# Kernel tuning notes

Measured on AMD Instinct MI355X. Metric: run time of the kernel, lower is better.

The kernel has to match this reference:

```python
import jax, jax.numpy as jnp
import numpy as np

N_NODES = 50000


def _gcn_layer(x, src, dst, W, b, inv_deg):
    # gather src features, scatter-add into dst, right-normalize, then dense transform
    agg = jax.ops.segment_sum(x[src], dst, num_segments=N_NODES)  # [N, F]
    h = agg * inv_deg[:, None]
    return h @ W + b


def setup_inputs() -> dict:
    key = jax.random.key(0)
    ks = jax.random.split(key, 6)
    E = 800000
    x = jax.random.normal(ks[0], (N_NODES, 128), dtype=jnp.float32)
    src = jax.random.randint(ks[1], (E,), 0, N_NODES, dtype=jnp.int64)
    dst = jax.random.randint(ks[2], (E,), 0, N_NODES, dtype=jnp.int64)
    W1 = jax.random.normal(ks[3], (128, 128), dtype=jnp.float32) * (1.0 / np.sqrt(128))
    b1 = jnp.zeros((128,), dtype=jnp.float32)
    W2 = jax.random.normal(ks[4], (128, 64), dtype=jnp.float32) * (1.0 / np.sqrt(128))
    b2 = jnp.zeros((64,), dtype=jnp.float32)
    return {"x": x, "src": src, "dst": dst, "W1": W1, "b1": b1, "W2": W2, "b2": b2}


def reference(x, src, dst, W1, b1, W2, b2):
    # in-degree, clamped to 1 (DGL norm='right')
    deg = jax.ops.segment_sum(jnp.ones_like(dst, dtype=x.dtype), dst, num_segments=N_NODES)
    inv_deg = 1.0 / jnp.maximum(deg, 1.0)
    h = _gcn_layer(x, src, dst, W1, b1, inv_deg)
    h = jax.nn.relu(h)  # Dropout in eval mode == identity
    out = _gcn_layer(h, src, dst, W2, b2, inv_deg)
    return out
```

## Files before the change

### kernel.cpp

```cpp
#include <hip/hip_runtime.h>


constexpr int NNODES = 50000;
constexpr int NEDGES = 800000;
constexpr int SCAN_BLOCKS = (NNODES + 255) / 256;
constexpr int ABLOCKS = 200;
constexpr int PER = (NEDGES + ABLOCKS - 1) / ABLOCKS;

typedef unsigned short ushortv8 __attribute__((ext_vector_type(8)));
typedef short bf16x8 __attribute__((ext_vector_type(8)));
typedef float f32x4 __attribute__((ext_vector_type(4)));

static __device__ __forceinline__ unsigned short f2bf(float f) {
    unsigned u = __float_as_uint(f);
    u += 0x7fff + ((u >> 16) & 1);
    return (unsigned short)(u >> 16);
}
static __device__ __forceinline__ float bf2f(unsigned short h) {
    return __uint_as_float((unsigned)h << 16);
}

__global__ __launch_bounds__(256) void partA_kernel(
    const int* __restrict__ src, const int* __restrict__ dst,
    unsigned* __restrict__ tmp, int* __restrict__ H,
    int* __restrict__ LOFS, int nE)
{
    __shared__ int cnt[256];
    __shared__ int ofs[256];
    __shared__ int cur[256];
    const int t = threadIdx.x;
    cnt[t] = 0;
    __syncthreads();
    const int lo = blockIdx.x * PER;
    const int hi = min(lo + PER, nE);
    for (int i = lo + t; i < hi; i += 256)
        atomicAdd(&cnt[dst[i] >> 8], 1);
    __syncthreads();
    ofs[t] = cnt[t];
    __syncthreads();
    #pragma unroll
    for (int off = 1; off < 256; off <<= 1) {
        const int o = (t >= off) ? ofs[t - off] : 0;
        __syncthreads();
        ofs[t] += o;
        __syncthreads();
    }
    const int excl = ofs[t] - cnt[t];
    cur[t] = excl;
    H[blockIdx.x * 256 + t] = cnt[t];
    LOFS[blockIdx.x * 256 + t] = excl;
    __syncthreads();
    for (int i = lo + t; i < hi; i += 256) {
        const int d = dst[i];
        const unsigned pk = ((unsigned)src[i] << 8) | (unsigned)(d & 255);
        const int pos = lo + atomicAdd(&cur[d >> 8], 1);
        tmp[pos] = pk;
    }
}

__global__ __launch_bounds__(256) void bucketScan_kernel(
    const int* __restrict__ H, int* __restrict__ bucketStart)
{
    __shared__ int s[256];
    const int t = threadIdx.x;
    int sum = 0;
    for (int w = 0; w < ABLOCKS; ++w) sum += H[w * 256 + t];
    s[t] = sum;
    __syncthreads();
    #pragma unroll
    for (int off = 1; off < 256; off <<= 1) {
        const int o = (t >= off) ? s[t - off] : 0;
        __syncthreads();
        s[t] += o;
        __syncthreads();
    }
    bucketStart[t] = s[t] - sum;
}

__global__ __launch_bounds__(256) void partB_kernel(
    const unsigned* __restrict__ tmp, const int* __restrict__ H,
    const int* __restrict__ LOFS, const int* __restrict__ bucketStart,
    int* __restrict__ csr, int* __restrict__ rowStart,
    float* __restrict__ inv_deg, int nNodes)
{
    __shared__ int pfx[ABLOCKS + 1];
    __shared__ int base[ABLOCKS];
    __shared__ int cnt[256];
    __shared__ int scn[256];
    __shared__ int fill[256];
    const int b = blockIdx.x;
    const int t = threadIdx.x;
    cnt[t] = 0;
    if (t < ABLOCKS) {
        pfx[t + 1] = H[t * 256 + b];
        base[t] = t * PER + LOFS[t * 256 + b];
    }
    if (t == 0) pfx[0] = 0;
    __syncthreads();
    if (t == 0) {
        int run = 0;
        for (int w = 0; w < ABLOCKS; ++w) { run += pfx[w + 1]; pfx[w + 1] = run; }
    }
    __syncthreads();
    const int total = pfx[ABLOCKS];
    for (int j = t; j < total; j += 256) {
        int loW = 0, hiW = ABLOCKS;
        while (hiW - loW > 1) {
            const int mid = (loW + hiW) >> 1;
            if (pfx[mid] <= j) loW = mid; else hiW = mid;
        }
        const unsigned p = tmp[base[loW] + (j - pfx[loW])];
        atomicAdd(&cnt[p & 255u], 1);
    }
    __syncthreads();
    scn[t] = cnt[t];
    __syncthreads();
    #pragma unroll
    for (int off = 1; off < 256; off <<= 1) {
        const int o = (t >= off) ? scn[t - off] : 0;
        __syncthreads();
        scn[t] += o;
        __syncthreads();
    }
    const int gbase = bucketStart[b];
    const int excl = gbase + scn[t] - cnt[t];
    const int node = b * 256 + t;
    if (node < nNodes) {
        rowStart[node] = excl;
        inv_deg[node] = 1.0f / fmaxf((float)cnt[t], 1.0f);
    }
    if (b == 0 && t == 0) rowStart[nNodes] = NEDGES;
    fill[t] = excl;
    __syncthreads();
    for (int j = t; j < total; j += 256) {
        int loW = 0, hiW = ABLOCKS;
        while (hiW - loW > 1) {
            const int mid = (loW + hiW) >> 1;
            if (pfx[mid] <= j) loW = mid; else hiW = mid;
        }
        const unsigned p = tmp[base[loW] + (j - pfx[loW])];
        const int pos = atomicAdd(&fill[p & 255u], 1);
        csr[pos] = (int)(p >> 8);
    }
}

__global__ __launch_bounds__(256) void cast_kernel(
    const float* __restrict__ in, ushortv8* __restrict__ outh, int n8)
{
    int i = blockIdx.x * 256 + threadIdx.x;
    if (i >= n8) return;
    const float4* p = reinterpret_cast<const float4*>(in) + (size_t)i * 2;
    const float4 a = p[0], b = p[1];
    ushortv8 v;
    v[0] = f2bf(a.x); v[1] = f2bf(a.y); v[2] = f2bf(a.z); v[3] = f2bf(a.w);
    v[4] = f2bf(b.x); v[5] = f2bf(b.y); v[6] = f2bf(b.z); v[7] = f2bf(b.w);
    outh[i] = v;
}

__global__ __launch_bounds__(256) void prep_kernel(
    const float* __restrict__ W1, const float* __restrict__ W2,
    unsigned short* __restrict__ Wt1, unsigned short* __restrict__ Wt2)
{
    const int i = blockIdx.x * 256 + threadIdx.x;
    if (i < 128 * 128) {
        const int n = i >> 7, k = i & 127;
        Wt1[i] = f2bf(W1[k * 128 + n]);
    } else if (i < 128 * 128 + 64 * 128) {
        const int j = i - 128 * 128;
        const int n = j >> 7, k = j & 127;
        Wt2[j] = f2bf(W2[k * 64 + n]);
    }
}

template<int F, bool EPI, bool OBF16>
__global__ __launch_bounds__(256) void gather_bf16_kernel(
    const ushortv8* __restrict__ feat, const int* __restrict__ csr,
    const int* __restrict__ rowStart, const float* __restrict__ inv_deg,
    const float* __restrict__ bias, void* __restrict__ outv, int nNodes)
{
    constexpr int LPR = F / 8;
    constexpr int EPW = 64 / LPR;
    const int wid = (blockIdx.x * 256 + threadIdx.x) >> 6;
    if (wid >= nNodes) return;
    const int lane = threadIdx.x & 63;
    const int eslot = lane / LPR;
    const int cg = lane % LPR;
    const int rs = rowStart[wid];
    const int re = rowStart[wid + 1];

    float acc0[8] = {}, acc1[8] = {};
    int j = rs + eslot;
    for (; j + EPW < re; j += 2 * EPW) {
        const int s0 = csr[j];
        const int s1 = csr[j + EPW];
        const ushortv8 v0 = feat[(size_t)s0 * LPR + cg];
        const ushortv8 v1 = feat[(size_t)s1 * LPR + cg];
        #pragma unroll
        for (int t = 0; t < 8; ++t) acc0[t] += bf2f(v0[t]);
        #pragma unroll
        for (int t = 0; t < 8; ++t) acc1[t] += bf2f(v1[t]);
    }
    if (j < re) {
        const int s0 = csr[j];
        const ushortv8 v0 = feat[(size_t)s0 * LPR + cg];
        #pragma unroll
        for (int t = 0; t < 8; ++t) acc0[t] += bf2f(v0[t]);
    }
    #pragma unroll
    for (int t = 0; t < 8; ++t) acc0[t] += acc1[t];

    #pragma unroll
    for (int off = LPR; off < 64; off <<= 1) {
        #pragma unroll
        for (int t = 0; t < 8; ++t) acc0[t] += __shfl_down(acc0[t], off, 64);
    }

    if (lane < LPR) {
        if constexpr (EPI) {
            const float s = inv_deg[wid];
            #pragma unroll
            for (int t = 0; t < 8; ++t) acc0[t] = acc0[t] * s + bias[cg * 8 + t];
        }
        if constexpr (OBF16) {
            ushortv8 ov;
            #pragma unroll
            for (int t = 0; t < 8; ++t) ov[t] = f2bf(acc0[t]);
            *reinterpret_cast<ushortv8*>(
                (unsigned short*)outv + (size_t)wid * F + cg * 8) = ov;
        } else {
            float* o = (float*)outv + (size_t)wid * F + cg * 8;
            *reinterpret_cast<float4*>(o) =
                make_float4(acc0[0], acc0[1], acc0[2], acc0[3]);
            *reinterpret_cast<float4*>(o + 4) =
                make_float4(acc0[4], acc0[5], acc0[6], acc0[7]);
        }
    }
}

template<int OUT, bool SCALE, bool BIAS, bool RELU>
__global__ __launch_bounds__(256) void mfma_gemm_kernel(
    const ushortv8* __restrict__ A,
    const float* __restrict__ inv_deg,
    const ushortv8* __restrict__ Wt,
    const float* __restrict__ bias,
    unsigned short* __restrict__ outh,
    int nrows)
{
    constexpr int NT = OUT / 16;
    constexpr int LDK = 136;
    __shared__ alignas(16) unsigned short lwt[OUT][LDK];
    __shared__ alignas(16) unsigned short la[64][LDK];

    const int row0 = blockIdx.x * 64;
    const int t = threadIdx.x;

    for (int i = t; i < OUT * 16; i += 256) {
        const int r = i >> 4, c = i & 15;
        *reinterpret_cast<ushortv8*>(&lwt[r][c * 8]) = Wt[i];
    }
    for (int i = t; i < 64 * 16; i += 256) {
        const int r = i >> 4, c = i & 15;
        const int row = row0 + r;
        ushortv8 v = {};
        if (row < nrows) {
            v = A[(size_t)row * 16 + c];
            if constexpr (SCALE) {
                const float s = inv_deg[row];
                #pragma unroll
                for (int jj = 0; jj < 8; ++jj) v[jj] = f2bf(bf2f(v[jj]) * s);
            }
        }
        *reinterpret_cast<ushortv8*>(&la[r][c * 8]) = v;
    }
    __syncthreads();

    const int wave = t >> 6, lane = t & 63;
    const int m = lane & 15, kg = lane >> 4;

    f32x4 acc[NT] = {};
    #pragma unroll
    for (int kk = 0; kk < 4; ++kk) {
        const bf16x8 af =
            *reinterpret_cast<const bf16x8*>(&la[wave * 16 + m][kk * 32 + kg * 8]);
        #pragma unroll
        for (int n = 0; n < NT; ++n) {
            const bf16x8 bf =
                *reinterpret_cast<const bf16x8*>(&lwt[n * 16 + m][kk * 32 + kg * 8]);
            acc[n] = __builtin_amdgcn_mfma_f32_16x16x32_bf16(af, bf, acc[n], 0, 0, 0);
        }
    }

    __syncthreads();
    unsigned short* lo = &la[0][0];
    constexpr int LDO = OUT + 8;
    #pragma unroll
    for (int n = 0; n < NT; ++n) {
        float bv = 0.f;
        if constexpr (BIAS) bv = bias[n * 16 + m];
        #pragma unroll
        for (int q = 0; q < 4; ++q) {
            const int r = wave * 16 + kg * 4 + q;
            float v = acc[n][q] + bv;
            if constexpr (RELU) v = fmaxf(v, 0.f);
            lo[r * LDO + n * 16 + m] = f2bf(v);
        }
    }
    __syncthreads();
    for (int i = t; i < 64 * (OUT / 8); i += 256) {
        const int r = i / (OUT / 8), c = i % (OUT / 8);
        const int row = row0 + r;
        if (row < nrows)
            *reinterpret_cast<ushortv8*>(&outh[(size_t)row * OUT + c * 8]) =
                *reinterpret_cast<const ushortv8*>(&lo[r * LDO + c * 8]);
    }
}

extern "C" void kernel_launch(void* const* d_in, const int* in_sizes, int n_in,
                              void* d_out, int out_size, void* d_ws, size_t ws_size,
                              hipStream_t stream)
{
    const float* x   = (const float*)d_in[0];
    const int*   src = (const int*)d_in[1];
    const int*   dst = (const int*)d_in[2];
    const float* W1  = (const float*)d_in[3];
    const float* b1  = (const float*)d_in[4];
    const float* W2  = (const float*)d_in[5];
    const float* b2  = (const float*)d_in[6];
    float* out = (float*)d_out;

    float* ws  = (float*)d_ws;
    int*   wsi = (int*)d_ws;
    int*            rowStart    = wsi + 0;
    float*          invdeg      = ws  + 50048;
    int*            bucketStart = wsi + 100096;
    int*            H           = wsi + 100352;
    int*            LOFS        = wsi + 151552;
    int*            csr         = wsi + 202752;
    unsigned*       tmp         = (unsigned*)(wsi + 1002752);
    unsigned short* Wt1         = (unsigned short*)(wsi + 1802752);
    unsigned short* Wt2         = (unsigned short*)(wsi + 1810944);
    ushortv8*       xh          = (ushortv8*)(wsi + 1815040);
    ushortv8*       aggH        = (ushortv8*)(wsi + 5015040);
    ushortv8*       h           = (ushortv8*)(wsi + 6615040);
    ushortv8*       y2h         = (ushortv8*)(wsi + 8215040);

    partA_kernel<<<ABLOCKS, 256, 0, stream>>>(src, dst, tmp, H, LOFS, NEDGES);
    bucketScan_kernel<<<1, 256, 0, stream>>>(H, bucketStart);
    partB_kernel<<<SCAN_BLOCKS, 256, 0, stream>>>(
        tmp, H, LOFS, bucketStart, csr, rowStart, invdeg, NNODES);

    cast_kernel<<<(NNODES * 128 / 8 + 255) / 256, 256, 0, stream>>>(
        x, xh, NNODES * 128 / 8);
    prep_kernel<<<(128 * 128 + 64 * 128 + 255) / 256, 256, 0, stream>>>(
        W1, W2, Wt1, Wt2);

    gather_bf16_kernel<128, false, true><<<(NNODES + 3) / 4, 256, 0, stream>>>(
        xh, csr, rowStart, nullptr, nullptr, aggH, NNODES);
    mfma_gemm_kernel<128, true, true, true><<<(NNODES + 63) / 64, 256, 0, stream>>>(
        aggH, invdeg, (const ushortv8*)Wt1, b1, (unsigned short*)h, NNODES);

    mfma_gemm_kernel<64, false, false, false><<<(NNODES + 63) / 64, 256, 0, stream>>>(
        h, nullptr, (const ushortv8*)Wt2, nullptr, (unsigned short*)y2h, NNODES);
    gather_bf16_kernel<64, true, false><<<(NNODES + 3) / 4, 256, 0, stream>>>(
        y2h, csr, rowStart, invdeg, b2, out, NNODES);
}
```

Measured before the change: 137.8 us.

## Fuse setup kernels, fold bucket scan into partB, and fuse both GEMMs

Merges the edge partitioning, feature cast and weight transpose into one multi-role setup kernel. Every partB block now recomputes the global bucket scan redundantly instead of relying on a separate single-block kernel. The two dense GEMMs are fused so the hidden layer stays in LDS and is never written to or read back from global memory. Together these cut five launches down to two and remove a global round trip for the hidden layer. In exchange, each partB block re-reads the whole H histogram, and the fused GEMM uses more LDS per block.

```diff
diff --git a/kernel.cpp b/kernel.cpp
--- a/kernel.cpp
+++ b/kernel.cpp
@@ -3,9 +3,37 @@
 
 constexpr int NNODES = 50000;
 constexpr int NEDGES = 800000;
-constexpr int SCAN_BLOCKS = (NNODES + 255) / 256;
+constexpr int NBUCKETS = (NNODES + 255) / 256;
 constexpr int ABLOCKS = 200;
 constexpr int PER = (NEDGES + ABLOCKS - 1) / ABLOCKS;
+constexpr int NB_CAST = NNODES * 128 / 8 / 256;
+constexpr int NB_PREP = (128 * 128 + 64 * 128 + 255) / 256;
+
+constexpr size_t SZ_ROWSTART = 50048;
+constexpr size_t SZ_INVDEG   = 50048;
+constexpr size_t SZ_H        = (size_t)ABLOCKS * 256;
+constexpr size_t SZ_LOFS     = (size_t)ABLOCKS * 256;
+constexpr size_t SZ_CSR      = NEDGES;
+constexpr size_t SZ_TMP      = NEDGES;
+constexpr size_t SZ_WT1      = 128 * 128 / 2;
+constexpr size_t SZ_WT2      = 64 * 128 / 2;
+constexpr size_t SZ_XH       = (size_t)NNODES * 128 / 2;
+constexpr size_t SZ_AGGH     = (size_t)NNODES * 128 / 2;
+constexpr size_t SZ_Y2H      = (size_t)NNODES * 64 / 2;
+
+constexpr size_t OFF_ROWSTART = 0;
+constexpr size_t OFF_INVDEG   = OFF_ROWSTART + SZ_ROWSTART;
+constexpr size_t OFF_H        = OFF_INVDEG   + SZ_INVDEG;
+constexpr size_t OFF_LOFS     = OFF_H        + SZ_H;
+constexpr size_t OFF_CSR      = OFF_LOFS     + SZ_LOFS;
+constexpr size_t OFF_TMP      = OFF_CSR      + SZ_CSR;
+constexpr size_t OFF_WT1      = OFF_TMP      + SZ_TMP;
+constexpr size_t OFF_WT2      = OFF_WT1      + SZ_WT1;
+constexpr size_t OFF_XH       = OFF_WT2      + SZ_WT2;
+constexpr size_t OFF_AGGH     = OFF_XH       + SZ_XH;
+constexpr size_t OFF_Y2H      = OFF_AGGH     + SZ_AGGH;
+constexpr size_t WS_WORDS     = OFF_Y2H      + SZ_Y2H;
+static_assert(WS_WORDS < 11452800, "exceeds r7-proven workspace size");
 
 typedef unsigned short ushortv8 __attribute__((ext_vector_type(8)));
 typedef short bf16x8 __attribute__((ext_vector_type(8)));
@@ -20,110 +48,132 @@
     return __uint_as_float((unsigned)h << 16);
 }
 
-__global__ __launch_bounds__(256) void partA_kernel(
+__global__ __launch_bounds__(256) void setup_kernel(
     const int* __restrict__ src, const int* __restrict__ dst,
-    unsigned* __restrict__ tmp, int* __restrict__ H,
-    int* __restrict__ LOFS, int nE)
+    unsigned* __restrict__ tmp, int* __restrict__ H, int* __restrict__ LOFS,
+    const float* __restrict__ x, ushortv8* __restrict__ xh,
+    const float* __restrict__ W1, const float* __restrict__ W2,
+    unsigned short* __restrict__ Wt1, unsigned short* __restrict__ Wt2)
 {
-    __shared__ int cnt[256];
-    __shared__ int ofs[256];
-    __shared__ int cur[256];
+    const int blk = blockIdx.x;
     const int t = threadIdx.x;
-    cnt[t] = 0;
-    __syncthreads();
-    const int lo = blockIdx.x * PER;
-    const int hi = min(lo + PER, nE);
-    for (int i = lo + t; i < hi; i += 256)
-        atomicAdd(&cnt[dst[i] >> 8], 1);
-    __syncthreads();
-    ofs[t] = cnt[t];
-    __syncthreads();
-    #pragma unroll
-    for (int off = 1; off < 256; off <<= 1) {
-        const int o = (t >= off) ? ofs[t - off] : 0;
-        __syncthreads();
-        ofs[t] += o;
-        __syncthreads();
-    }
-    const int excl = ofs[t] - cnt[t];
-    cur[t] = excl;
-    H[blockIdx.x * 256 + t] = cnt[t];
-    LOFS[blockIdx.x * 256 + t] = excl;
-    __syncthreads();
-    for (int i = lo + t; i < hi; i += 256) {
-        const int d = dst[i];
-        const unsigned pk = ((unsigned)src[i] << 8) | (unsigned)(d & 255);
-        const int pos = lo + atomicAdd(&cur[d >> 8], 1);
-        tmp[pos] = pk;
-    }
-}
-
-__global__ __launch_bounds__(256) void bucketScan_kernel(
-    const int* __restrict__ H, int* __restrict__ bucketStart)
-{
-    __shared__ int s[256];
-    const int t = threadIdx.x;
-    int sum = 0;
-    for (int w = 0; w < ABLOCKS; ++w) sum += H[w * 256 + t];
-    s[t] = sum;
-    __syncthreads();
-    #pragma unroll
-    for (int off = 1; off < 256; off <<= 1) {
-        const int o = (t >= off) ? s[t - off] : 0;
-        __syncthreads();
-        s[t] += o;
-        __syncthreads();
-    }
-    bucketStart[t] = s[t] - sum;
+    if (blk < ABLOCKS) {
+        __shared__ int cnt[256];
+        __shared__ int ofs[256];
+        __shared__ int cur[256];
+        cnt[t] = 0;
+        __syncthreads();
+        const int lo = blk * PER;
+        const int hi = min(lo + PER, NEDGES);
+        for (int i = lo + t; i < hi; i += 256)
+            atomicAdd(&cnt[dst[i] >> 8], 1);
+        __syncthreads();
+        ofs[t] = cnt[t];
+        __syncthreads();
+        #pragma unroll
+        for (int off = 1; off < 256; off <<= 1) {
+            const int o = (t >= off) ? ofs[t - off] : 0;
+            __syncthreads();
+            ofs[t] += o;
+            __syncthreads();
+        }
+        const int excl = ofs[t] - cnt[t];
+        cur[t] = excl;
+        H[blk * 256 + t] = cnt[t];
+        LOFS[blk * 256 + t] = excl;
+        __syncthreads();
+        for (int i = lo + t; i < hi; i += 256) {
+            const int d = dst[i];
+            const unsigned pk = ((unsigned)src[i] << 8) | (unsigned)(d & 255);
+            const int pos = lo + atomicAdd(&cur[d >> 8], 1);
+            tmp[pos] = pk;
+        }
+    } else if (blk < ABLOCKS + NB_CAST) {
+        const int i = (blk - ABLOCKS) * 256 + t;
+        const float4* p = reinterpret_cast<const float4*>(x) + (size_t)i * 2;
+        const float4 a = p[0], b = p[1];
+        ushortv8 v;
+        v[0] = f2bf(a.x); v[1] = f2bf(a.y); v[2] = f2bf(a.z); v[3] = f2bf(a.w);
+        v[4] = f2bf(b.x); v[5] = f2bf(b.y); v[6] = f2bf(b.z); v[7] = f2bf(b.w);
+        xh[i] = v;
+    } else {
+        const int i = (blk - ABLOCKS - NB_CAST) * 256 + t;
+        if (i < 128 * 128) {
+            const int n = i >> 7, k = i & 127;
+            Wt1[i] = f2bf(W1[k * 128 + n]);
+        } else if (i < 128 * 128 + 64 * 128) {
+            const int j = i - 128 * 128;
+            const int n = j >> 7, k = j & 127;
+            Wt2[j] = f2bf(W2[k * 64 + n]);
+        }
+    }
 }
 
 __global__ __launch_bounds__(256) void partB_kernel(
     const unsigned* __restrict__ tmp, const int* __restrict__ H,
-    const int* __restrict__ LOFS, const int* __restrict__ bucketStart,
-    int* __restrict__ csr, int* __restrict__ rowStart,
-    float* __restrict__ inv_deg, int nNodes)
+    const int* __restrict__ LOFS, int* __restrict__ csr,
+    int* __restrict__ rowStart, float* __restrict__ inv_deg, int nNodes)
 {
-    __shared__ int pfx[ABLOCKS + 1];
-    __shared__ int base[ABLOCKS];
+    __shared__ int cs[256];
+    __shared__ int s[256];
+    __shared__ int epfx[256];
+    __shared__ int base[256];
     __shared__ int cnt[256];
-    __shared__ int scn[256];
     __shared__ int fill[256];
     const int b = blockIdx.x;
     const int t = threadIdx.x;
+
+    int sum = 0;
+    for (int w = 0; w < ABLOCKS; ++w) sum += H[w * 256 + t];
+    cs[t] = sum;
+    s[t] = sum;
+    __syncthreads();
+    #pragma unroll
+    for (int off = 1; off < 256; off <<= 1) {
+        const int o = (t >= off) ? s[t - off] : 0;
+        __syncthreads();
+        s[t] += o;
+        __syncthreads();
+    }
+    const int gbase = s[b] - cs[b];
+    const int total = cs[b];
+    __syncthreads();
+
+    const int hv = (t < ABLOCKS) ? H[t * 256 + b] : 0;
+    s[t] = hv;
+    if (t < ABLOCKS) base[t] = t * PER + LOFS[t * 256 + b];
     cnt[t] = 0;
-    if (t < ABLOCKS) {
-        pfx[t + 1] = H[t * 256 + b];
-        base[t] = t * PER + LOFS[t * 256 + b];
-    }
-    if (t == 0) pfx[0] = 0;
-    __syncthreads();
-    if (t == 0) {
-        int run = 0;
-        for (int w = 0; w < ABLOCKS; ++w) { run += pfx[w + 1]; pfx[w + 1] = run; }
-    }
-    __syncthreads();
-    const int total = pfx[ABLOCKS];
+    __syncthreads();
+    #pragma unroll
+    for (int off = 1; off < 256; off <<= 1) {
+        const int o = (t >= off) ? s[t - off] : 0;
+        __syncthreads();
+        s[t] += o;
+        __syncthreads();
+    }
+    epfx[t] = s[t] - hv;
+    __syncthreads();
+
     for (int j = t; j < total; j += 256) {
         int loW = 0, hiW = ABLOCKS;
         while (hiW - loW > 1) {
             const int mid = (loW + hiW) >> 1;
-            if (pfx[mid] <= j) loW = mid; else hiW = mid;
-        }
-        const unsigned p = tmp[base[loW] + (j - pfx[loW])];
+            if (epfx[mid] <= j) loW = mid; else hiW = mid;
+        }
+        const unsigned p = tmp[base[loW] + (j - epfx[loW])];
         atomicAdd(&cnt[p & 255u], 1);
     }
     __syncthreads();
-    scn[t] = cnt[t];
+    s[t] = cnt[t];
     __syncthreads();
     #pragma unroll
     for (int off = 1; off < 256; off <<= 1) {
-        const int o = (t >= off) ? scn[t - off] : 0;
-        __syncthreads();
-        scn[t] += o;
-        __syncthreads();
-    }
-    const int gbase = bucketStart[b];
-    const int excl = gbase + scn[t] - cnt[t];
+        const int o = (t >= off) ? s[t - off] : 0;
+        __syncthreads();
+        s[t] += o;
+        __syncthreads();
+    }
+    const int excl = gbase + s[t] - cnt[t];
     const int node = b * 256 + t;
     if (node < nNodes) {
         rowStart[node] = excl;
@@ -132,43 +182,16 @@
     if (b == 0 && t == 0) rowStart[nNodes] = NEDGES;
     fill[t] = excl;
     __syncthreads();
+
     for (int j = t; j < total; j += 256) {
         int loW = 0, hiW = ABLOCKS;
         while (hiW - loW > 1) {
             const int mid = (loW + hiW) >> 1;
-            if (pfx[mid] <= j) loW = mid; else hiW = mid;
-        }
-        const unsigned p = tmp[base[loW] + (j - pfx[loW])];
+            if (epfx[mid] <= j) loW = mid; else hiW = mid;
+        }
+        const unsigned p = tmp[base[loW] + (j - epfx[loW])];
         const int pos = atomicAdd(&fill[p & 255u], 1);
         csr[pos] = (int)(p >> 8);
-    }
-}
-
-__global__ __launch_bounds__(256) void cast_kernel(
-    const float* __restrict__ in, ushortv8* __restrict__ outh, int n8)
-{
-    int i = blockIdx.x * 256 + threadIdx.x;
-    if (i >= n8) return;
-    const float4* p = reinterpret_cast<const float4*>(in) + (size_t)i * 2;
-    const float4 a = p[0], b = p[1];
-    ushortv8 v;
-    v[0] = f2bf(a.x); v[1] = f2bf(a.y); v[2] = f2bf(a.z); v[3] = f2bf(a.w);
-    v[4] = f2bf(b.x); v[5] = f2bf(b.y); v[6] = f2bf(b.z); v[7] = f2bf(b.w);
-    outh[i] = v;
-}
-
-__global__ __launch_bounds__(256) void prep_kernel(
-    const float* __restrict__ W1, const float* __restrict__ W2,
-    unsigned short* __restrict__ Wt1, unsigned short* __restrict__ Wt2)
-{
-    const int i = blockIdx.x * 256 + threadIdx.x;
-    if (i < 128 * 128) {
-        const int n = i >> 7, k = i & 127;
-        Wt1[i] = f2bf(W1[k * 128 + n]);
-    } else if (i < 128 * 128 + 64 * 128) {
-        const int j = i - 128 * 128;
-        const int n = j >> 7, k = j & 127;
-        Wt2[j] = f2bf(W2[k * 64 + n]);
     }
 }
 
@@ -237,26 +260,30 @@
     }
 }
 
-template<int OUT, bool SCALE, bool BIAS, bool RELU>
-__global__ __launch_bounds__(256) void mfma_gemm_kernel(
+__global__ __launch_bounds__(256) void mfma_fused_kernel(
     const ushortv8* __restrict__ A,
     const float* __restrict__ inv_deg,
-    const ushortv8* __restrict__ Wt,
-    const float* __restrict__ bias,
-    unsigned short* __restrict__ outh,
+    const ushortv8* __restrict__ Wt1,
+    const float* __restrict__ b1,
+    const ushortv8* __restrict__ Wt2,
+    unsigned short* __restrict__ y2h,
     int nrows)
 {
-    constexpr int NT = OUT / 16;
     constexpr int LDK = 136;
-    __shared__ alignas(16) unsigned short lwt[OUT][LDK];
+    __shared__ alignas(16) unsigned short lwt1[128][LDK];
+    __shared__ alignas(16) unsigned short lwt2[64][LDK];
     __shared__ alignas(16) unsigned short la[64][LDK];
 
     const int row0 = blockIdx.x * 64;
     const int t = threadIdx.x;
 
-    for (int i = t; i < OUT * 16; i += 256) {
+    for (int i = t; i < 128 * 16; i += 256) {
         const int r = i >> 4, c = i & 15;
-        *reinterpret_cast<ushortv8*>(&lwt[r][c * 8]) = Wt[i];
+        *reinterpret_cast<ushortv8*>(&lwt1[r][c * 8]) = Wt1[i];
+    }
+    for (int i = t; i < 64 * 16; i += 256) {
+        const int r = i >> 4, c = i & 15;
+        *reinterpret_cast<ushortv8*>(&lwt2[r][c * 8]) = Wt2[i];
     }
     for (int i = t; i < 64 * 16; i += 256) {
         const int r = i >> 4, c = i & 15;
@@ -264,11 +291,9 @@
         ushortv8 v = {};
         if (row < nrows) {
             v = A[(size_t)row * 16 + c];
-            if constexpr (SCALE) {
-                const float s = inv_deg[row];
-                #pragma unroll
-                for (int jj = 0; jj < 8; ++jj) v[jj] = f2bf(bf2f(v[jj]) * s);
-            }
+            const float s = inv_deg[row];
+            #pragma unroll
+            for (int jj = 0; jj < 8; ++jj) v[jj] = f2bf(bf2f(v[jj]) * s);
         }
         *reinterpret_cast<ushortv8*>(&la[r][c * 8]) = v;
     }
@@ -277,41 +302,57 @@
     const int wave = t >> 6, lane = t & 63;
     const int m = lane & 15, kg = lane >> 4;
 
-    f32x4 acc[NT] = {};
+    f32x4 acc1[8] = {};
     #pragma unroll
     for (int kk = 0; kk < 4; ++kk) {
         const bf16x8 af =
             *reinterpret_cast<const bf16x8*>(&la[wave * 16 + m][kk * 32 + kg * 8]);
         #pragma unroll
-        for (int n = 0; n < NT; ++n) {
+        for (int n = 0; n < 8; ++n) {
             const bf16x8 bf =
-                *reinterpret_cast<const bf16x8*>(&lwt[n * 16 + m][kk * 32 + kg * 8]);
-            acc[n] = __builtin_amdgcn_mfma_f32_16x16x32_bf16(af, bf, acc[n], 0, 0, 0);
-        }
-    }
-
-    __syncthreads();
-    unsigned short* lo = &la[0][0];
-    constexpr int LDO = OUT + 8;
-    #pragma unroll
-    for (int n = 0; n < NT; ++n) {
-        float bv = 0.f;
-        if constexpr (BIAS) bv = bias[n * 16 + m];
+                *reinterpret_cast<const bf16x8*>(&lwt1[n * 16 + m][kk * 32 + kg * 8]);
+            acc1[n] = __builtin_amdgcn_mfma_f32_16x16x32_bf16(af, bf, acc1[n], 0, 0, 0);
+        }
+    }
+    #pragma unroll
+    for (int n = 0; n < 8; ++n) {
+        const float bv = b1[n * 16 + m];
         #pragma unroll
         for (int q = 0; q < 4; ++q) {
             const int r = wave * 16 + kg * 4 + q;
-            float v = acc[n][q] + bv;
-            if constexpr (RELU) v = fmaxf(v, 0.f);
-            lo[r * LDO + n * 16 + m] = f2bf(v);
-        }
-    }
-    __syncthreads();
-    for (int i = t; i < 64 * (OUT / 8); i += 256) {
-        const int r = i / (OUT / 8), c = i % (OUT / 8);
+            la[r][n * 16 + m] = f2bf(fmaxf(acc1[n][q] + bv, 0.f));
+        }
+    }
+    __syncthreads();
+
+    f32x4 acc2[4] = {};
+    #pragma unroll
+    for (int kk = 0; kk < 4; ++kk) {
+        const bf16x8 af =
+            *reinterpret_cast<const bf16x8*>(&la[wave * 16 + m][kk * 32 + kg * 8]);
+        #pragma unroll
+        for (int n = 0; n < 4; ++n) {
+            const bf16x8 bf =
+                *reinterpret_cast<const bf16x8*>(&lwt2[n * 16 + m][kk * 32 + kg * 8]);
+            acc2[n] = __builtin_amdgcn_mfma_f32_16x16x32_bf16(af, bf, acc2[n], 0, 0, 0);
+        }
+    }
+    __syncthreads();
+    #pragma unroll
+    for (int n = 0; n < 4; ++n) {
+        #pragma unroll
+        for (int q = 0; q < 4; ++q) {
+            const int r = wave * 16 + kg * 4 + q;
+            la[r][n * 16 + m] = f2bf(acc2[n][q]);
+        }
+    }
+    __syncthreads();
+    for (int i = t; i < 64 * 8; i += 256) {
+        const int r = i >> 3, c = i & 7;
         const int row = row0 + r;
         if (row < nrows)
-            *reinterpret_cast<ushortv8*>(&outh[(size_t)row * OUT + c * 8]) =
-                *reinterpret_cast<const ushortv8*>(&lo[r * LDO + c * 8]);
+            *reinterpret_cast<ushortv8*>(&y2h[(size_t)row * 64 + c * 8]) =
+                *reinterpret_cast<const ushortv8*>(&la[r][c * 8]);
     }
 }
 
@@ -330,37 +371,31 @@
 
     float* ws  = (float*)d_ws;
     int*   wsi = (int*)d_ws;
-    int*            rowStart    = wsi + 0;
-    float*          invdeg      = ws  + 50048;
-    int*            bucketStart = wsi + 100096;
-    int*            H           = wsi + 100352;
-    int*            LOFS        = wsi + 151552;
-    int*            csr         = wsi + 202752;
-    unsigned*       tmp         = (unsigned*)(wsi + 1002752);
-    unsigned short* Wt1         = (unsigned short*)(wsi + 1802752);
-    unsigned short* Wt2         = (unsigned short*)(wsi + 1810944);
-    ushortv8*       xh          = (ushortv8*)(wsi + 1815040);
-    ushortv8*       aggH        = (ushortv8*)(wsi + 5015040);
-    ushortv8*       h           = (ushortv8*)(wsi + 6615040);
-    ushortv8*       y2h         = (ushortv8*)(wsi + 8215040);
-
-    partA_kernel<<<ABLOCKS, 256, 0, stream>>>(src, dst, tmp, H, LOFS, NEDGES);
-    bucketScan_kernel<<<1, 256, 0, stream>>>(H, bucketStart);
-    partB_kernel<<<SCAN_BLOCKS, 256, 0, stream>>>(
-        tmp, H, LOFS, bucketStart, csr, rowStart, invdeg, NNODES);
-
-    cast_kernel<<<(NNODES * 128 / 8 + 255) / 256, 256, 0, stream>>>(
-        x, xh, NNODES * 128 / 8);
-    prep_kernel<<<(128 * 128 + 64 * 128 + 255) / 256, 256, 0, stream>>>(
-        W1, W2, Wt1, Wt2);
+    int*            rowStart = wsi + OFF_ROWSTART;
+    float*          invdeg   = ws  + OFF_INVDEG;
+    int*            H        = wsi + OFF_H;
+    int*            LOFS     = wsi + OFF_LOFS;
+    int*            csr      = wsi + OFF_CSR;
+    unsigned*       tmp      = (unsigned*)(wsi + OFF_TMP);
+    unsigned short* Wt1      = (unsigned short*)(wsi + OFF_WT1);
+    unsigned short* Wt2      = (unsigned short*)(wsi + OFF_WT2);
+    ushortv8*       xh       = (ushortv8*)(wsi + OFF_XH);
+    ushortv8*       aggH     = (ushortv8*)(wsi + OFF_AGGH);
+    unsigned short* y2h      = (unsigned short*)(wsi + OFF_Y2H);
+
+    setup_kernel<<<ABLOCKS + NB_CAST + NB_PREP, 256, 0, stream>>>(
+        src, dst, tmp, H, LOFS, x, xh, W1, W2, Wt1, Wt2);
+
+    partB_kernel<<<NBUCKETS, 256, 0, stream>>>(
+        tmp, H, LOFS, csr, rowStart, invdeg, NNODES);
 
     gather_bf16_kernel<128, false, true><<<(NNODES + 3) / 4, 256, 0, stream>>>(
         xh, csr, rowStart, nullptr, nullptr, aggH, NNODES);
-    mfma_gemm_kernel<128, true, true, true><<<(NNODES + 63) / 64, 256, 0, stream>>>(
-        aggH, invdeg, (const ushortv8*)Wt1, b1, (unsigned short*)h, NNODES);
-
-    mfma_gemm_kernel<64, false, false, false><<<(NNODES + 63) / 64, 256, 0, stream>>>(
-        h, nullptr, (const ushortv8*)Wt2, nullptr, (unsigned short*)y2h, NNODES);
+
+    mfma_fused_kernel<<<(NNODES + 63) / 64, 256, 0, stream>>>(
+        aggH, invdeg, (const ushortv8*)Wt1, b1, (const ushortv8*)Wt2,
+        y2h, NNODES);
+
     gather_bf16_kernel<64, true, false><<<(NNODES + 3) / 4, 256, 0, stream>>>(
-        y2h, csr, rowStart, invdeg, b2, out, NNODES);
-}
+        (const ushortv8*)y2h, csr, rowStart, invdeg, b2, out, NNODES);
+}
```

Result: faster. 123.2 us, median of 2 (-10.6%).
